# Optimization experiments

Measured on AMD Instinct MI355X. Metric: run time of the kernel, lower is better.

## Reference

```python
import jax, jax.numpy as jnp
import numpy as np

N_NODES = 50000
N_EDGES = 800000
D_IN = 128
D_HID = 128
D_OUT = 128


def _sage_conv(x, row, col, Wl, Wr, b):
    # PyG SAGEConv (mean aggregation, root weight, bias):
    # out = mean_{j in N(i)} x_j @ Wl^T + x_i @ Wr^T + b
    n = x.shape[0]
    msg = x[col]                                            # [E, D] gather from source nodes
    agg = jax.ops.segment_sum(msg, row, num_segments=n)     # [N, D]
    deg = jax.ops.segment_sum(jnp.ones((row.shape[0],), x.dtype), row, num_segments=n)
    agg = agg / jnp.maximum(deg, 1.0)[:, None]
    return agg @ Wl.T + x @ Wr.T + b


def setup_inputs() -> dict:
    key = jax.random.key(0)
    ks = jax.random.split(key, 12)
    x = jax.random.normal(ks[0], (N_NODES, D_IN), dtype=jnp.float32)
    edge_row = jax.random.randint(ks[1], (N_EDGES,), 0, N_NODES)
    edge_col = jax.random.randint(ks[2], (N_EDGES,), 0, N_NODES)
    dims = [(D_HID, D_IN), (D_HID, D_HID), (D_OUT, D_HID)]
    inp = {"x": x, "edge_row": edge_row, "edge_col": edge_col}
    for i, (do, di) in enumerate(dims):
        s = 1.0 / np.sqrt(di)
        inp[f"Wl{i}"] = jax.random.uniform(ks[3 + 3 * i], (do, di), jnp.float32, -s, s)
        inp[f"Wr{i}"] = jax.random.uniform(ks[4 + 3 * i], (do, di), jnp.float32, -s, s)
        inp[f"b{i}"] = jax.random.uniform(ks[5 + 3 * i], (do,), jnp.float32, -s, s)
    return inp


def reference(x, edge_row, edge_col, Wl0, Wr0, b0, Wl1, Wr1, b1, Wl2, Wr2, b2):
    # Single branch (num_layers=[3]), use_res=True, dropout=0 (eval mode).
    params = [(Wl0, Wr0, b0), (Wl1, Wr1, b1), (Wl2, Wr2, b2)]
    x1 = _sage_conv(x, edge_row, edge_col, *params[0])
    for Wl, Wr, b in params[1:]:
        x2 = x1
        x1 = jax.nn.relu(x1)
        x1 = _sage_conv(x1, edge_row, edge_col, Wl, Wr, b) + x2
    # x_final = sum(branches) / number; one branch -> divide by 1
    return x1 / 1.0
```

## Files before the change

### kernel.cpp

```cpp
#include <hip/hip_runtime.h>

#define NN 50000
#define NE 800000
#define D  128

typedef _Float16 f16;
typedef _Float16 f16x4 __attribute__((ext_vector_type(4)));
typedef _Float16 f16x8 __attribute__((ext_vector_type(8)));
typedef float f32x4 __attribute__((ext_vector_type(4)));
typedef unsigned short u16;

__global__ __launch_bounds__(256) void prep(
    const float* __restrict__ x, f16* __restrict__ xf,
    const float* w0, const float* w1, const float* w2,
    const float* w3, const float* w4, const float* w5,
    f16* d0, f16* d1, f16* d2, f16* d3, f16* d4, f16* d5,
    int* __restrict__ deg) {
    int b = blockIdx.x;
    if (b < 6250) {
        int i = b * 256 + threadIdx.x;
        float4 v = ((const float4*)x)[i];
        f16x4 o = {(f16)v.x, (f16)v.y, (f16)v.z, (f16)v.w};
        ((f16x4*)xf)[i] = o;
    } else if (b < 6346) {
        int wb = b - 6250;
        int mat = wb >> 4;
        const float* s; f16* d;
        switch (mat) {
            case 0: s = w0; d = d0; break; case 1: s = w1; d = d1; break;
            case 2: s = w2; d = d2; break; case 3: s = w3; d = d3; break;
            case 4: s = w4; d = d4; break; default: s = w5; d = d5; break;
        }
        int i = (wb & 15) * 256 + threadIdx.x;
        float4 v = ((const float4*)s)[i];
        f16x4 o = {(f16)v.x, (f16)v.y, (f16)v.z, (f16)v.w};
        ((f16x4*)d)[i] = o;
    } else {
        int i = (b - 6346) * 256 + threadIdx.x;
        if (i < NN) deg[i] = 0;
    }
}


__global__ __launch_bounds__(256) void count_deg_rank(
    const int* __restrict__ row, int* __restrict__ deg, u16* __restrict__ rank, int e) {
    int i = blockIdx.x * blockDim.x + threadIdx.x;
    if (i < e) rank[i] = (u16)atomicAdd(&deg[row[i]], 1);
}

__global__ void scan_partial(const int* __restrict__ deg, int* __restrict__ bsum, int n) {
    __shared__ int s[1024];
    int i = blockIdx.x * 1024 + threadIdx.x;
    s[threadIdx.x] = (i < n) ? deg[i] : 0;
    __syncthreads();
    for (int off = 512; off > 0; off >>= 1) {
        if (threadIdx.x < off) s[threadIdx.x] += s[threadIdx.x + off];
        __syncthreads();
    }
    if (threadIdx.x == 0) bsum[blockIdx.x] = s[0];
}

__global__ void scan_final(const int* __restrict__ deg, const int* __restrict__ bsum,
                           int* __restrict__ offsets, int n, int nb) {
    __shared__ int s[1024];
    __shared__ int base;
    if (threadIdx.x < 64) {
        int t = threadIdx.x;
        int v = (t < nb && t < (int)blockIdx.x) ? bsum[t] : 0;
#pragma unroll
        for (int m = 1; m < 64; m <<= 1) v += __shfl_xor(v, m, 64);
        if (t == 0) base = v;
    }
    int i = blockIdx.x * 1024 + threadIdx.x;
    int dv = (i < n) ? deg[i] : 0;
    s[threadIdx.x] = dv;
    __syncthreads();
    for (int off = 1; off < 1024; off <<= 1) {
        int t = (threadIdx.x >= (unsigned)off) ? s[threadIdx.x - off] : 0;
        __syncthreads();
        s[threadIdx.x] += t;
        __syncthreads();
    }
    if (i < n) {
        offsets[i + 1] = s[threadIdx.x] + base;
        if (i == 0) offsets[0] = 0;
    }
}

__global__ __launch_bounds__(256) void fill_csr(
    const int* __restrict__ row, const int* __restrict__ col,
    const u16* __restrict__ rank, const int* __restrict__ offsets,
    u16* __restrict__ csr_col, int e) {
    int i = blockIdx.x * blockDim.x + threadIdx.x;
    if (i < e) {
        int p = offsets[row[i]] + (int)rank[i];
        csr_col[p] = (u16)col[i];
    }
}

template<int RELU>
__global__ __launch_bounds__(256) void aggregate_f16(
    const f16* __restrict__ h, const int* __restrict__ offsets,
    const u16* __restrict__ csr, f16* __restrict__ agg) {
    int node = blockIdx.x * 4 + (threadIdx.x >> 6);
    int lane = threadIdx.x & 63;
    int sub = lane >> 4, fl = lane & 15;
    int s0 = offsets[node], e0 = offsets[node + 1];
    int deg = e0 - s0;

    float acc[8];
#pragma unroll
    for (int u = 0; u < 8; ++u) acc[u] = 0.f;

    int j = s0 + sub;

#define ACCUM(cidx)                                                        \
    do {                                                                   \
        f16x8 v = *(const f16x8*)(h + (size_t)(cidx) * D + fl * 8);        \
        if (RELU) {                                                        \
            _Pragma("unroll")                                              \
            for (int u = 0; u < 8; ++u)                                    \
                v[u] = (v[u] < (f16)0) ? (f16)0 : v[u];                    \
        }                                                                  \
        _Pragma("unroll")                                                  \
        for (int u = 0; u < 8; ++u)                                        \
            acc[u] = fmaf((float)v[u], 1.0f, acc[u]);                      \
    } while (0)

    for (int it = deg >> 3; it > 0; --it, j += 8) {
        int c0 = csr[j];
        int c1 = csr[j + 4];
        f16x8 v0 = *(const f16x8*)(h + (size_t)c0 * D + fl * 8);
        f16x8 v1 = *(const f16x8*)(h + (size_t)c1 * D + fl * 8);
        if (RELU) {
#pragma unroll
            for (int u = 0; u < 8; ++u) {
                v0[u] = (v0[u] < (f16)0) ? (f16)0 : v0[u];
                v1[u] = (v1[u] < (f16)0) ? (f16)0 : v1[u];
            }
        }
#pragma unroll
        for (int u = 0; u < 8; ++u) {
            acc[u] = fmaf((float)v0[u], 1.0f, acc[u]);
            acc[u] = fmaf((float)v1[u], 1.0f, acc[u]);
        }
    }
    if (deg & 4) {
        int c = csr[j];
        ACCUM(c);
        j += 4;
    }
    if (sub < (deg & 3)) {
        int c = csr[j];
        ACCUM(c);
    }
#undef ACCUM

#pragma unroll
    for (int u = 0; u < 8; ++u) {
        acc[u] += __shfl_xor(acc[u], 16, 64);
        acc[u] += __shfl_xor(acc[u], 32, 64);
    }
    if (sub == 0) {
        float inv = 1.f / fmaxf((float)deg, 1.f);
        f16x8 o;
#pragma unroll
        for (int u = 0; u < 8; ++u) o[u] = (f16)(acc[u] * inv);
        *((f16x8*)(agg + (size_t)node * D) + fl) = o;
    }
}

#define WPAD 72

template<int RELU_X, int ADD_RES, int OUT_F32>
__global__ __launch_bounds__(256, 4) void sage_gemm_mfma(
    const f16* __restrict__ aggb, const f16* __restrict__ xb,
    const f16* __restrict__ Wl, const f16* __restrict__ Wr,
    const float* __restrict__ bias, float* __restrict__ outf,
    f16* __restrict__ outh) {
    __shared__ f16 sW[2][128][WPAD];

    const int tid  = threadIdx.x;
    const int wave = tid >> 6;
    const int lane = tid & 63;
    const int lm = lane & 15;
    const int q  = lane >> 4;
    const int mt = blockIdx.x * 64 + wave * 16;

    int row = mt + lm;
    int rclamp = (row < NN) ? row : NN - 1;

    f16x8 Aa[4], Ax[4];
    const f16* arow = aggb + (size_t)rclamp * D + q * 8;
    const f16* xrow = xb  + (size_t)rclamp * D + q * 8;
#pragma unroll
    for (int ks = 0; ks < 4; ++ks) {
        Aa[ks] = *(const f16x8*)(arow + ks * 32);
        f16x8 v = *(const f16x8*)(xrow + ks * 32);
        if (RELU_X) {
#pragma unroll
            for (int u = 0; u < 8; ++u) v[u] = (v[u] < (f16)0) ? (f16)0 : v[u];
        }
        Ax[ks] = v;
    }

    f32x4 acc[8];
#pragma unroll
    for (int nt = 0; nt < 8; ++nt) acc[nt] = (f32x4){0.f, 0.f, 0.f, 0.f};

    for (int p = 0; p < 2; ++p) {
        __syncthreads();
#pragma unroll
        for (int it = 0; it < 8; ++it) {
            int idx = tid + it * 256;
            int mat = idx >> 10;
            int n   = (idx >> 3) & 127;
            int c   = idx & 7;
            const f16* W = mat ? Wr : Wl;
            f16x8 v = *(const f16x8*)(W + n * D + p * 64 + c * 8);
            *(f16x8*)&sW[mat][n][c * 8] = v;
        }
        __syncthreads();

#pragma unroll
        for (int nt = 0; nt < 8; ++nt) {
#pragma unroll
            for (int k2 = 0; k2 < 2; ++k2) {
                f16x8 bl = *(const f16x8*)&sW[0][nt * 16 + lm][k2 * 32 + q * 8];
                acc[nt] = __builtin_amdgcn_mfma_f32_16x16x32_f16(Aa[p * 2 + k2], bl, acc[nt], 0, 0, 0);
                f16x8 br = *(const f16x8*)&sW[1][nt * 16 + lm][k2 * 32 + q * 8];
                acc[nt] = __builtin_amdgcn_mfma_f32_16x16x32_f16(Ax[p * 2 + k2], br, acc[nt], 0, 0, 0);
            }
        }
    }

#pragma unroll
    for (int nt = 0; nt < 8; ++nt) {
        int n = nt * 16 + lm;
        float bval = bias[n];
#pragma unroll
        for (int r = 0; r < 4; ++r) {
            int m = mt + q * 4 + r;
            if (m < NN) {
                size_t idx = (size_t)m * D + n;
                float v = acc[nt][r] + bval;
                if (ADD_RES) v += (float)xb[idx];
                if (OUT_F32) outf[idx] = v;
                else         outh[idx] = (f16)v;
            }
        }
    }
}


extern "C" void kernel_launch(void* const* d_in, const int* in_sizes, int n_in,
                              void* d_out, int out_size, void* d_ws, size_t ws_size,
                              hipStream_t stream) {
    const float* x    = (const float*)d_in[0];
    const int*   erow = (const int*)d_in[1];
    const int*   ecol = (const int*)d_in[2];
    const float* Wl0 = (const float*)d_in[3];
    const float* Wr0 = (const float*)d_in[4];
    const float* b0  = (const float*)d_in[5];
    const float* Wl1 = (const float*)d_in[6];
    const float* Wr1 = (const float*)d_in[7];
    const float* b1  = (const float*)d_in[8];
    const float* Wl2 = (const float*)d_in[9];
    const float* Wr2 = (const float*)d_in[10];
    const float* b2  = (const float*)d_in[11];

    char* ws = (char*)d_ws;
    size_t off = 0;
    auto carve = [&](size_t bytes) -> void* {
        void* p = ws + off;
        off = (off + bytes + 255) & ~(size_t)255;
        return p;
    };
    int*   deg     = (int*)carve((size_t)NN * 4);
    int*   offsets = (int*)carve((size_t)(NN + 1) * 4);
    int*   bsum    = (int*)carve(64 * 4);
    u16*   rank    = (u16*)carve((size_t)NE * 2);
    u16*   csr_col = (u16*)carve((size_t)NE * 2);
    f16*   xf      = (f16*)carve((size_t)NN * D * 2);
    f16*   x1      = (f16*)carve((size_t)NN * D * 2);
    f16*   aggb    = (f16*)carve((size_t)NN * D * 2);
    f16*   wl0 = (f16*)carve(D * D * 2); f16* wr0 = (f16*)carve(D * D * 2);
    f16*   wl1 = (f16*)carve(D * D * 2); f16* wr1 = (f16*)carve(D * D * 2);
    f16*   wl2 = (f16*)carve(D * D * 2); f16* wr2 = (f16*)carve(D * D * 2);
    (void)ws_size; (void)in_sizes; (void)n_in; (void)out_size;

    float* outp = (float*)d_out;

    prep<<<6542, 256, 0, stream>>>(x, xf, Wl0, Wr0, Wl1, Wr1, Wl2, Wr2,
                                   wl0, wr0, wl1, wr1, wl2, wr2, deg);

    count_deg_rank<<<(NE + 255) / 256, 256, 0, stream>>>(erow, deg, rank, NE);
    const int nsb = (NN + 1023) / 1024;
    scan_partial<<<nsb, 1024, 0, stream>>>(deg, bsum, NN);
    scan_final<<<nsb, 1024, 0, stream>>>(deg, bsum, offsets, NN, nsb);
    fill_csr<<<(NE + 255) / 256, 256, 0, stream>>>(erow, ecol, rank, offsets, csr_col, NE);

    const int agrid = NN / 4;
    const int ggrid = (NN + 63) / 64;

    aggregate_f16<0><<<agrid, 256, 0, stream>>>(xf, offsets, csr_col, aggb);
    sage_gemm_mfma<0, 0, 0><<<ggrid, 256, 0, stream>>>(aggb, xf, wl0, wr0, b0,
                                                       nullptr, x1);
    aggregate_f16<1><<<agrid, 256, 0, stream>>>(x1, offsets, csr_col, aggb);
    sage_gemm_mfma<1, 1, 0><<<ggrid, 256, 0, stream>>>(aggb, x1, wl1, wr1, b1,
                                                       nullptr, x1);
    aggregate_f16<1><<<agrid, 256, 0, stream>>>(x1, offsets, csr_col, aggb);
    sage_gemm_mfma<1, 1, 1><<<ggrid, 256, 0, stream>>>(aggb, x1, wl2, wr2, b2,
                                                       outp, nullptr);
}
```

Before: 289.2 us.

## Map one node per quarter-wave in aggregation, vectorize CSR build, prefetch GEMM weights

Aggregation now assigns one node to each 16-lane quarter-wave instead of four edges per node across a wave. This removes the cross-lane shuffle reduction and lets all lanes store, but quarters loop to the wave's maximum degree and accumulate in fp16 vectors rather than fp32, so precision drops. The CSR count and fill kernels process two edges per thread with int2 loads. The GEMM loads both weight halves into registers ahead of the LDS stores, which drops one barrier and overlaps global loads with compute.

```diff
diff --git a/kernel.cpp b/kernel.cpp
--- a/kernel.cpp
+++ b/kernel.cpp
@@ -43,9 +43,14 @@
 
 
 __global__ __launch_bounds__(256) void count_deg_rank(
-    const int* __restrict__ row, int* __restrict__ deg, u16* __restrict__ rank, int e) {
+    const int* __restrict__ row, int* __restrict__ deg, u16* __restrict__ rank, int e2) {
     int i = blockIdx.x * blockDim.x + threadIdx.x;
-    if (i < e) rank[i] = (u16)atomicAdd(&deg[row[i]], 1);
+    if (i < e2) {
+        int2 r = ((const int2*)row)[i];
+        unsigned ra = (unsigned)atomicAdd(&deg[r.x], 1);
+        unsigned rb = (unsigned)atomicAdd(&deg[r.y], 1);
+        ((unsigned*)rank)[i] = (ra & 0xffffu) | (rb << 16);
+    }
 }
 
 __global__ void scan_partial(const int* __restrict__ deg, int* __restrict__ bsum, int n) {
@@ -90,11 +95,14 @@
 __global__ __launch_bounds__(256) void fill_csr(
     const int* __restrict__ row, const int* __restrict__ col,
     const u16* __restrict__ rank, const int* __restrict__ offsets,
-    u16* __restrict__ csr_col, int e) {
+    u16* __restrict__ csr_col, int e2) {
     int i = blockIdx.x * blockDim.x + threadIdx.x;
-    if (i < e) {
-        int p = offsets[row[i]] + (int)rank[i];
-        csr_col[p] = (u16)col[i];
+    if (i < e2) {
+        int2 r = ((const int2*)row)[i];
+        int2 c = ((const int2*)col)[i];
+        unsigned rk = ((const unsigned*)rank)[i];
+        csr_col[offsets[r.x] + (int)(rk & 0xffffu)] = (u16)c.x;
+        csr_col[offsets[r.y] + (int)(rk >> 16)]     = (u16)c.y;
     }
 }
 
@@ -102,36 +110,31 @@
 __global__ __launch_bounds__(256) void aggregate_f16(
     const f16* __restrict__ h, const int* __restrict__ offsets,
     const u16* __restrict__ csr, f16* __restrict__ agg) {
-    int node = blockIdx.x * 4 + (threadIdx.x >> 6);
+    int wave = threadIdx.x >> 6;
     int lane = threadIdx.x & 63;
     int sub = lane >> 4, fl = lane & 15;
-    int s0 = offsets[node], e0 = offsets[node + 1];
-    int deg = e0 - s0;
-
-    float acc[8];
-#pragma unroll
-    for (int u = 0; u < 8; ++u) acc[u] = 0.f;
-
-    int j = s0 + sub;
-
-#define ACCUM(cidx)                                                        \
-    do {                                                                   \
-        f16x8 v = *(const f16x8*)(h + (size_t)(cidx) * D + fl * 8);        \
-        if (RELU) {                                                        \
-            _Pragma("unroll")                                              \
-            for (int u = 0; u < 8; ++u)                                    \
-                v[u] = (v[u] < (f16)0) ? (f16)0 : v[u];                    \
-        }                                                                  \
-        _Pragma("unroll")                                                  \
-        for (int u = 0; u < 8; ++u)                                        \
-            acc[u] = fmaf((float)v[u], 1.0f, acc[u]);                      \
-    } while (0)
-
-    for (int it = deg >> 3; it > 0; --it, j += 8) {
-        int c0 = csr[j];
-        int c1 = csr[j + 4];
-        f16x8 v0 = *(const f16x8*)(h + (size_t)c0 * D + fl * 8);
-        f16x8 v1 = *(const f16x8*)(h + (size_t)c1 * D + fl * 8);
+    int node = blockIdx.x * 16 + wave * 4 + sub;
+    int s0 = offsets[node];
+    int dg = offsets[node + 1] - s0;
+
+    int maxd = dg;
+    maxd = max(maxd, __shfl_xor(maxd, 16, 64));
+    maxd = max(maxd, __shfl_xor(maxd, 32, 64));
+
+    f16x8 acc = {};
+    const f16* hp = h + fl * 8;
+
+    int it = 0;
+    for (; it + 2 <= maxd; it += 2) {
+        f16x8 v0 = {}, v1 = {};
+        if (it < dg) {
+            int c0 = (int)csr[s0 + it];
+            v0 = *(const f16x8*)(hp + (size_t)c0 * D);
+        }
+        if (it + 1 < dg) {
+            int c1 = (int)csr[s0 + it + 1];
+            v1 = *(const f16x8*)(hp + (size_t)c1 * D);
+        }
         if (RELU) {
 #pragma unroll
             for (int u = 0; u < 8; ++u) {
@@ -139,35 +142,27 @@
                 v1[u] = (v1[u] < (f16)0) ? (f16)0 : v1[u];
             }
         }
-#pragma unroll
-        for (int u = 0; u < 8; ++u) {
-            acc[u] = fmaf((float)v0[u], 1.0f, acc[u]);
-            acc[u] = fmaf((float)v1[u], 1.0f, acc[u]);
-        }
-    }
-    if (deg & 4) {
-        int c = csr[j];
-        ACCUM(c);
-        j += 4;
-    }
-    if (sub < (deg & 3)) {
-        int c = csr[j];
-        ACCUM(c);
-    }
-#undef ACCUM
-
-#pragma unroll
-    for (int u = 0; u < 8; ++u) {
-        acc[u] += __shfl_xor(acc[u], 16, 64);
-        acc[u] += __shfl_xor(acc[u], 32, 64);
-    }
-    if (sub == 0) {
-        float inv = 1.f / fmaxf((float)deg, 1.f);
-        f16x8 o;
-#pragma unroll
-        for (int u = 0; u < 8; ++u) o[u] = (f16)(acc[u] * inv);
-        *((f16x8*)(agg + (size_t)node * D) + fl) = o;
-    }
+        acc = acc + v0;
+        acc = acc + v1;
+    }
+    if (it < maxd) {
+        f16x8 v0 = {};
+        if (it < dg) {
+            int c0 = (int)csr[s0 + it];
+            v0 = *(const f16x8*)(hp + (size_t)c0 * D);
+        }
+        if (RELU) {
+#pragma unroll
+            for (int u = 0; u < 8; ++u) v0[u] = (v0[u] < (f16)0) ? (f16)0 : v0[u];
+        }
+        acc = acc + v0;
+    }
+
+    float inv = 1.f / fmaxf((float)dg, 1.f);
+    f16x8 o;
+#pragma unroll
+    for (int u = 0; u < 8; ++u) o[u] = (f16)((float)acc[u] * inv);
+    *((f16x8*)(agg + (size_t)node * D) + fl) = o;
 }
 
 #define WPAD 72
@@ -204,24 +199,38 @@
         Ax[ks] = v;
     }
 
+    f16x8 st[8];
+#pragma unroll
+    for (int it = 0; it < 8; ++it) {
+        int idx = tid + it * 256;
+        int mat = idx >> 10, n = (idx >> 3) & 127, c = idx & 7;
+        const f16* W = mat ? Wr : Wl;
+        st[it] = *(const f16x8*)(W + n * D + c * 8);
+    }
+
     f32x4 acc[8];
 #pragma unroll
     for (int nt = 0; nt < 8; ++nt) acc[nt] = (f32x4){0.f, 0.f, 0.f, 0.f};
 
+#pragma unroll
     for (int p = 0; p < 2; ++p) {
-        __syncthreads();
+        if (p) __syncthreads();
 #pragma unroll
         for (int it = 0; it < 8; ++it) {
             int idx = tid + it * 256;
-            int mat = idx >> 10;
-            int n   = (idx >> 3) & 127;
-            int c   = idx & 7;
-            const f16* W = mat ? Wr : Wl;
-            f16x8 v = *(const f16x8*)(W + n * D + p * 64 + c * 8);
-            *(f16x8*)&sW[mat][n][c * 8] = v;
+            int mat = idx >> 10, n = (idx >> 3) & 127, c = idx & 7;
+            *(f16x8*)&sW[mat][n][c * 8] = st[it];
         }
         __syncthreads();
-
+        if (p == 0) {
+#pragma unroll
+            for (int it = 0; it < 8; ++it) {
+                int idx = tid + it * 256;
+                int mat = idx >> 10, n = (idx >> 3) & 127, c = idx & 7;
+                const f16* W = mat ? Wr : Wl;
+                st[it] = *(const f16x8*)(W + n * D + 64 + c * 8);
+            }
+        }
 #pragma unroll
         for (int nt = 0; nt < 8; ++nt) {
 #pragma unroll
@@ -294,13 +303,14 @@
     prep<<<6542, 256, 0, stream>>>(x, xf, Wl0, Wr0, Wl1, Wr1, Wl2, Wr2,
                                    wl0, wr0, wl1, wr1, wl2, wr2, deg);
 
-    count_deg_rank<<<(NE + 255) / 256, 256, 0, stream>>>(erow, deg, rank, NE);
+    const int e2 = NE / 2;
+    count_deg_rank<<<(e2 + 255) / 256, 256, 0, stream>>>(erow, deg, rank, e2);
     const int nsb = (NN + 1023) / 1024;
     scan_partial<<<nsb, 1024, 0, stream>>>(deg, bsum, NN);
     scan_final<<<nsb, 1024, 0, stream>>>(deg, bsum, offsets, NN, nsb);
-    fill_csr<<<(NE + 255) / 256, 256, 0, stream>>>(erow, ecol, rank, offsets, csr_col, NE);
-
-    const int agrid = NN / 4;
+    fill_csr<<<(e2 + 255) / 256, 256, 0, stream>>>(erow, ecol, rank, offsets, csr_col, e2);
+
+    const int agrid = NN / 16;
     const int ggrid = (NN + 63) / 64;
 
     aggregate_f16<0><<<agrid, 256, 0, stream>>>(xf, offsets, csr_col, aggb);
```

New measurement: 305.5 us. 5.6% more time.
